# Optimization experiments

Measured on AMD Instinct MI355X. Metric: run time of the kernel, lower is better.

Reference implementation:

```python
import jax, jax.numpy as jnp
import numpy as np

EPS = 1e-08


def _center(K):
    # H K H with H = I - 11^T/n, expressed as O(n^2) double mean-subtraction
    rm = K.mean(axis=-1, keepdims=True)
    cm = K.mean(axis=-2, keepdims=True)
    tm = K.mean(axis=(-1, -2), keepdims=True)
    return K - rm - cm + tm


def setup_inputs() -> dict:
    key = jax.random.key(0)
    k1, k2 = jax.random.split(key)
    L, B, n, d = 5, 8, 1024, 64
    teacher = jax.random.normal(k1, (L, B, n, d), dtype=jnp.float32)
    student = jax.random.normal(k2, (L, B, n, d), dtype=jnp.float32)
    return {"teacher": teacher, "student": student}


def reference(teacher, student):
    # teacher, student: [L, B, n, d]  (internal=True, dim>=3 branch)
    cX = _center(jnp.einsum('lbnd,lbmd->lbnm', teacher, teacher))  # [L,B,n,n]
    cY = _center(jnp.einsum('lbnd,lbmd->lbnm', student, student))  # [L,B,n,n]
    hsic_xy = jnp.sum(cX * cY, axis=(-1, -2))  # [L,B]
    var_x = jnp.sqrt(jnp.sum(cX * cX, axis=(-1, -2)))  # [L,B]
    var_y = jnp.sqrt(jnp.sum(cY * cY, axis=(-1, -2)))  # [L,B]
    ratio = jnp.abs(hsic_xy / (var_x * var_y))  # [L,B]
    loss_per_layer = -jnp.log(ratio.mean(axis=-1) + EPS)  # [L]
    return loss_per_layer.mean()  # sum over layers / length
```

## Files before the change

### kernel.cpp

```cpp
#include <hip/hip_runtime.h>
#include <math.h>

#define LL 5
#define BB 8
#define NN 1024
#define DD 64
#define LB 40
#define SPLIT 16
#define KC (NN / SPLIT)
#define ZC (2 * DD)
#define NQ 3

#define GP_SHORTS (LB * SPLIT * NQ * 4096)
#define GP_FLOATS (GP_SHORTS / 2)
#define SP_OFF GP_FLOATS
#define ACC_OFF (GP_FLOATS + LB * SPLIT * ZC)

typedef short short8 __attribute__((ext_vector_type(8)));
typedef float floatx4 __attribute__((ext_vector_type(4)));

__device__ __forceinline__ unsigned short f2bf(float f) {
    union { float f; unsigned u; } v; v.f = f;
    const unsigned u = v.u;
    return (unsigned short)((u + 0x7FFFu + ((u >> 16) & 1u)) >> 16);
}
__device__ __forceinline__ float bf2f(unsigned short h) {
    union { unsigned u; float f; } v; v.u = ((unsigned)h) << 16; return v.f;
}
__device__ __forceinline__ float bflo(unsigned u) {
    union { unsigned u; float f; } v; v.u = u << 16; return v.f;
}
__device__ __forceinline__ float bfhi(unsigned u) {
    union { unsigned u; float f; } v; v.u = u & 0xFFFF0000u; return v.f;
}

__device__ __forceinline__ short8 read_frag(const short* Zt, int tbase, int lane, int k0) {
    const int c = tbase + (lane & 15);
    const int o = (k0 >> 3) + (lane >> 4);
    const int oct = (o ^ ((c + (c >> 4)) & 15)) & 7;
    return *(const short8*)(Zt + c * 64 + (oct << 3));
}

__global__ __launch_bounds__(256) void gram_kernel(const float* __restrict__ X,
                                                   const float* __restrict__ Y,
                                                   unsigned* __restrict__ Gp,
                                                   float* __restrict__ Sp) {
    __shared__ short Zt[ZC * KC];
    __shared__ float cscr[8][ZC];

    const int lb = blockIdx.y, nc = blockIdx.x, tid = threadIdx.x;
    const int r0 = nc * KC;
    const float4* X4 = (const float4*)(X + (size_t)lb * NN * DD);
    const float4* Y4 = (const float4*)(Y + (size_t)lb * NN * DD);

    const int col4 = tid & 31;
    const int rb = tid >> 5;
    float4 v[8];
#pragma unroll
    for (int m = 0; m < 8; ++m) {
        const int row = 8 * rb + m;
        v[m] = (col4 < 16) ? X4[(size_t)(r0 + row) * 16 + col4]
                           : Y4[(size_t)(r0 + row) * 16 + (col4 - 16)];
    }

#pragma unroll
    for (int e = 0; e < 4; ++e) {
        const int c = 4 * col4 + e;
        short8 w8;
        float cs = 0.f;
#pragma unroll
        for (int m = 0; m < 8; ++m) {
            const float fv = (e == 0) ? v[m].x : (e == 1) ? v[m].y : (e == 2) ? v[m].z : v[m].w;
            const unsigned short b = f2bf(fv);
            cs += bf2f(b);
            w8[m] = (short)b;
        }
        const int oct = (rb ^ ((c + (c >> 4)) & 15)) & 7;
        *(short8*)(Zt + c * 64 + (oct << 3)) = w8;
        cscr[rb][c] = cs;
    }
    __syncthreads();
    if (tid < ZC) {
        float s = 0.f;
#pragma unroll
        for (int g = 0; g < 8; ++g) s += cscr[g][tid];
        Sp[(lb * SPLIT + nc) * ZC + tid] = s;
    }

    const int lane = tid & 63, w = tid >> 6;
    const int jbeg = (w < 2) ? 0 : 4;

    floatx4 acc[2][8];
#pragma unroll
    for (int i = 0; i < 2; ++i)
#pragma unroll
        for (int j = 0; j < 8; ++j) acc[i][j] = (floatx4){0.f, 0.f, 0.f, 0.f};

#pragma unroll
    for (int k0 = 0; k0 < KC; k0 += 32) {
        short8 af[2], bfr[8];
#pragma unroll
        for (int i = 0; i < 2; ++i) af[i] = read_frag(Zt, (2 * w + i) * 16, lane, k0);
#pragma unroll
        for (int j = 0; j < 8; ++j)
            if (j >= jbeg) bfr[j] = read_frag(Zt, j * 16, lane, k0);
#pragma unroll
        for (int i = 0; i < 2; ++i)
#pragma unroll
            for (int j = 0; j < 8; ++j)
                if (j >= jbeg)
                    acc[i][j] = __builtin_amdgcn_mfma_f32_16x16x32_bf16(af[i], bfr[j], acc[i][j], 0, 0, 0);
    }

    unsigned* Gb = Gp + (size_t)(lb * SPLIT + nc) * (NQ * 2048);
    const int g = lane >> 4, cl = lane & 15;
#pragma unroll
    for (int i = 0; i < 2; ++i)
#pragma unroll
        for (int j = 0; j < 8; ++j) {
            if (j < jbeg) continue;
            const int slab = (w < 2) ? ((j < 4) ? 0 : 1) : 2;
            const int qrow0 = (w < 2 ? (2 * w + i) : (2 * (w - 2) + i)) * 16 + g * 4;
            const int qcol = (j & 3) * 16 + cl;
            const unsigned lo = (unsigned)f2bf(acc[i][j][0]) | ((unsigned)f2bf(acc[i][j][1]) << 16);
            const unsigned hi = (unsigned)f2bf(acc[i][j][2]) | ((unsigned)f2bf(acc[i][j][3]) << 16);
            Gb[slab * 2048 + (qrow0 >> 1) * 64 + qcol] = lo;
            Gb[slab * 2048 + ((qrow0 >> 1) + 1) * 64 + qcol] = hi;
        }
}

__global__ __launch_bounds__(256) void reduce_kernel(const unsigned* __restrict__ Gp,
                                                     const float* __restrict__ Sp,
                                                     float* __restrict__ Acc2) {
    const int b = blockIdx.x;
    const int lb = b / (NQ * 4);
    const int rem = b % (NQ * 4);
    const int q = rem >> 2, seg = rem & 3;
    const int tid = threadIdx.x;

    __shared__ float stot[ZC];
    __shared__ float red[4];

    if (tid < ZC) {
        float s = 0.f;
#pragma unroll
        for (int sp = 0; sp < SPLIT; ++sp) s += Sp[(lb * SPLIT + sp) * ZC + tid];
        stot[tid] = s;
    }
    __syncthreads();

    const int u0 = seg * 512 + tid * 2;
    const int rp = u0 >> 6;
    const int c0 = u0 & 63;

    float g00 = 0.f, g10 = 0.f, g01 = 0.f, g11 = 0.f;
#pragma unroll
    for (int sp = 0; sp < SPLIT; ++sp) {
        const uint2 p = *(const uint2*)&Gp[((size_t)(lb * SPLIT + sp) * NQ + q) * 2048 + u0];
        g00 += bflo(p.x); g10 += bfhi(p.x);
        g01 += bflo(p.y); g11 += bfhi(p.y);
    }
    const int rowbase = (q == 2) ? 64 : 0;
    const int colbase = (q == 0) ? 0 : 64;
    const float inv_n = 1.0f / (float)NN;
    const float sr0 = stot[rowbase + 2 * rp] * inv_n;
    const float sr1 = stot[rowbase + 2 * rp + 1] * inv_n;
    const float sc0 = stot[colbase + c0];
    const float sc1 = stot[colbase + c0 + 1];
    float sq = 0.f;
    { const float cv = g00 - sr0 * sc0; sq += cv * cv; }
    { const float cv = g10 - sr1 * sc0; sq += cv * cv; }
    { const float cv = g01 - sr0 * sc1; sq += cv * cv; }
    { const float cv = g11 - sr1 * sc1; sq += cv * cv; }

#pragma unroll
    for (int off = 32; off; off >>= 1) sq += __shfl_down(sq, off);
    const int wave = tid >> 6;
    if ((tid & 63) == 0) red[wave] = sq;
    __syncthreads();
    if (tid == 0)
        Acc2[lb * 12 + q * 4 + seg] = red[0] + red[1] + red[2] + red[3];
}

__global__ void final_kernel(const float* __restrict__ Acc2, float* __restrict__ out) {
    const int tid = threadIdx.x;
    float v = 0.0f;
    if (tid < LB) {
        float vxx = 0.f, hxy = 0.f, vyy = 0.f;
#pragma unroll
        for (int s = 0; s < 4; ++s) {
            vxx += Acc2[tid * 12 + s];
            hxy += Acc2[tid * 12 + 4 + s];
            vyy += Acc2[tid * 12 + 8 + s];
        }
        v = fabsf(hxy / (sqrtf(vxx) * sqrtf(vyy)));
    }
    v += __shfl_xor(v, 1);
    v += __shfl_xor(v, 2);
    v += __shfl_xor(v, 4);
    float loss = 0.0f;
#pragma unroll
    for (int l = 0; l < LL; ++l) {
        const float sl = __shfl(v, l * BB);
        loss += -logf(sl * (1.0f / (float)BB) + 1e-8f);
    }
    if (tid == 0) out[0] = loss * (1.0f / (float)LL);
}

extern "C" void kernel_launch(void* const* d_in, const int* in_sizes, int n_in,
                              void* d_out, int out_size, void* d_ws, size_t ws_size,
                              hipStream_t stream) {
    const float* teacher = (const float*)d_in[0];
    const float* student = (const float*)d_in[1];
    float* ws = (float*)d_ws;
    unsigned* Gp = (unsigned*)ws;
    float* Sp = ws + SP_OFF;
    float* Acc2 = ws + ACC_OFF;

    dim3 grid1(SPLIT, LB);
    gram_kernel<<<grid1, 256, 0, stream>>>(teacher, student, Gp, Sp);
    reduce_kernel<<<LB * NQ * 4, 256, 0, stream>>>(Gp, Sp, Acc2);
    final_kernel<<<1, 64, 0, stream>>>(Acc2, (float*)d_out);
}
```

Before: 78.99 us.

## Halve split count, store fp32 MFMA fragments, fold final kernel into reduce

```diff
diff --git a/kernel.cpp b/kernel.cpp
--- a/kernel.cpp
+++ b/kernel.cpp
@@ -6,15 +6,15 @@
 #define NN 1024
 #define DD 64
 #define LB 40
-#define SPLIT 16
-#define KC (NN / SPLIT)
-#define ZC (2 * DD)
-#define NQ 3
-
-#define GP_SHORTS (LB * SPLIT * NQ * 4096)
-#define GP_FLOATS (GP_SHORTS / 2)
-#define SP_OFF GP_FLOATS
-#define ACC_OFF (GP_FLOATS + LB * SPLIT * ZC)
+#define SPLIT 8
+#define KC 128
+#define ZC 128
+#define PF_PER 12288
+
+#define SP_OFF 0
+#define ACC_OFF (LB * SPLIT * ZC)
+#define CNT_OFF (ACC_OFF + LB * 3)
+#define P_OFF (ACC_OFF + 128)
 
 typedef short short8 __attribute__((ext_vector_type(8)));
 typedef float floatx4 __attribute__((ext_vector_type(4)));
@@ -27,31 +27,27 @@
 __device__ __forceinline__ float bf2f(unsigned short h) {
     union { unsigned u; float f; } v; v.u = ((unsigned)h) << 16; return v.f;
 }
-__device__ __forceinline__ float bflo(unsigned u) {
-    union { unsigned u; float f; } v; v.u = u << 16; return v.f;
-}
-__device__ __forceinline__ float bfhi(unsigned u) {
-    union { unsigned u; float f; } v; v.u = u & 0xFFFF0000u; return v.f;
-}
 
 __device__ __forceinline__ short8 read_frag(const short* Zt, int tbase, int lane, int k0) {
     const int c = tbase + (lane & 15);
     const int o = (k0 >> 3) + (lane >> 4);
-    const int oct = (o ^ ((c + (c >> 4)) & 15)) & 7;
-    return *(const short8*)(Zt + c * 64 + (oct << 3));
-}
-
-__global__ __launch_bounds__(256) void gram_kernel(const float* __restrict__ X,
+    const int oct = (o ^ ((c + (c >> 4)) & 15)) & 15;
+    return *(const short8*)(Zt + c * KC + (oct << 3));
+}
+
+__global__ __launch_bounds__(512) void gram_kernel(const float* __restrict__ X,
                                                    const float* __restrict__ Y,
-                                                   unsigned* __restrict__ Gp,
-                                                   float* __restrict__ Sp) {
+                                                   float* __restrict__ ws) {
     __shared__ short Zt[ZC * KC];
-    __shared__ float cscr[8][ZC];
-
-    const int lb = blockIdx.y, nc = blockIdx.x, tid = threadIdx.x;
-    const int r0 = nc * KC;
+    __shared__ float cscr[16][ZC];
+
+    const int lb = blockIdx.y, sp = blockIdx.x, tid = threadIdx.x;
+    const int r0 = sp * KC;
     const float4* X4 = (const float4*)(X + (size_t)lb * NN * DD);
     const float4* Y4 = (const float4*)(Y + (size_t)lb * NN * DD);
+
+    if (blockIdx.x == 0 && blockIdx.y == 0 && tid < 128)
+        ((unsigned*)(ws + ACC_OFF))[tid] = 0u;
 
     const int col4 = tid & 31;
     const int rb = tid >> 5;
@@ -75,136 +71,129 @@
             cs += bf2f(b);
             w8[m] = (short)b;
         }
-        const int oct = (rb ^ ((c + (c >> 4)) & 15)) & 7;
-        *(short8*)(Zt + c * 64 + (oct << 3)) = w8;
+        const int oct = (rb ^ ((c + (c >> 4)) & 15)) & 15;
+        *(short8*)(Zt + c * KC + (oct << 3)) = w8;
         cscr[rb][c] = cs;
     }
     __syncthreads();
     if (tid < ZC) {
         float s = 0.f;
 #pragma unroll
-        for (int g = 0; g < 8; ++g) s += cscr[g][tid];
-        Sp[(lb * SPLIT + nc) * ZC + tid] = s;
+        for (int g = 0; g < 16; ++g) s += cscr[g][tid];
+        ws[SP_OFF + (lb * SPLIT + sp) * ZC + tid] = s;
     }
 
     const int lane = tid & 63, w = tid >> 6;
-    const int jbeg = (w < 2) ? 0 : 4;
-
-    floatx4 acc[2][8];
-#pragma unroll
-    for (int i = 0; i < 2; ++i)
-#pragma unroll
-        for (int j = 0; j < 8; ++j) acc[i][j] = (floatx4){0.f, 0.f, 0.f, 0.f};
+    const int jbeg = (w < 4) ? 0 : 4;
+
+    floatx4 acc[8];
+#pragma unroll
+    for (int j = 0; j < 8; ++j) acc[j] = (floatx4){0.f, 0.f, 0.f, 0.f};
 
 #pragma unroll
     for (int k0 = 0; k0 < KC; k0 += 32) {
-        short8 af[2], bfr[8];
-#pragma unroll
-        for (int i = 0; i < 2; ++i) af[i] = read_frag(Zt, (2 * w + i) * 16, lane, k0);
+        const short8 af = read_frag(Zt, 16 * w, lane, k0);
+        short8 bfr[8];
 #pragma unroll
         for (int j = 0; j < 8; ++j)
-            if (j >= jbeg) bfr[j] = read_frag(Zt, j * 16, lane, k0);
-#pragma unroll
-        for (int i = 0; i < 2; ++i)
-#pragma unroll
-            for (int j = 0; j < 8; ++j)
-                if (j >= jbeg)
-                    acc[i][j] = __builtin_amdgcn_mfma_f32_16x16x32_bf16(af[i], bfr[j], acc[i][j], 0, 0, 0);
-    }
-
-    unsigned* Gb = Gp + (size_t)(lb * SPLIT + nc) * (NQ * 2048);
-    const int g = lane >> 4, cl = lane & 15;
-#pragma unroll
-    for (int i = 0; i < 2; ++i)
-#pragma unroll
-        for (int j = 0; j < 8; ++j) {
-            if (j < jbeg) continue;
-            const int slab = (w < 2) ? ((j < 4) ? 0 : 1) : 2;
-            const int qrow0 = (w < 2 ? (2 * w + i) : (2 * (w - 2) + i)) * 16 + g * 4;
-            const int qcol = (j & 3) * 16 + cl;
-            const unsigned lo = (unsigned)f2bf(acc[i][j][0]) | ((unsigned)f2bf(acc[i][j][1]) << 16);
-            const unsigned hi = (unsigned)f2bf(acc[i][j][2]) | ((unsigned)f2bf(acc[i][j][3]) << 16);
-            Gb[slab * 2048 + (qrow0 >> 1) * 64 + qcol] = lo;
-            Gb[slab * 2048 + ((qrow0 >> 1) + 1) * 64 + qcol] = hi;
-        }
-}
-
-__global__ __launch_bounds__(256) void reduce_kernel(const unsigned* __restrict__ Gp,
-                                                     const float* __restrict__ Sp,
-                                                     float* __restrict__ Acc2) {
+            if (j >= jbeg) bfr[j] = read_frag(Zt, 16 * j, lane, k0);
+#pragma unroll
+        for (int j = 0; j < 8; ++j)
+            if (j >= jbeg)
+                acc[j] = __builtin_amdgcn_mfma_f32_16x16x32_bf16(af, bfr[j], acc[j], 0, 0, 0);
+    }
+
+    float* Pb = ws + P_OFF + (size_t)(lb * SPLIT + sp) * PF_PER;
+#pragma unroll
+    for (int j = 0; j < 8; ++j) {
+        if (j < jbeg) continue;
+        const int q = (w < 4) ? ((j < 4) ? 0 : 1) : 2;
+        const int ti = (w < 4) ? w : (w - 4);
+        const int t = ti * 4 + (j & 3);
+        *(floatx4*)(Pb + ((q * 16 + t) * 64 + lane) * 4) = acc[j];
+    }
+}
+
+__global__ __launch_bounds__(256) void reduce_kernel(float* __restrict__ ws,
+                                                     float* __restrict__ out) {
     const int b = blockIdx.x;
-    const int lb = b / (NQ * 4);
-    const int rem = b % (NQ * 4);
+    const int lb = b / 12;
+    const int rem = b % 12;
     const int q = rem >> 2, seg = rem & 3;
     const int tid = threadIdx.x;
 
-    __shared__ float stot[ZC];
+    __shared__ float Sl[ZC];
     __shared__ float red[4];
+    __shared__ unsigned lastflag;
 
     if (tid < ZC) {
         float s = 0.f;
 #pragma unroll
-        for (int sp = 0; sp < SPLIT; ++sp) s += Sp[(lb * SPLIT + sp) * ZC + tid];
-        stot[tid] = s;
-    }
-    __syncthreads();
-
-    const int u0 = seg * 512 + tid * 2;
-    const int rp = u0 >> 6;
-    const int c0 = u0 & 63;
-
-    float g00 = 0.f, g10 = 0.f, g01 = 0.f, g11 = 0.f;
-#pragma unroll
-    for (int sp = 0; sp < SPLIT; ++sp) {
-        const uint2 p = *(const uint2*)&Gp[((size_t)(lb * SPLIT + sp) * NQ + q) * 2048 + u0];
-        g00 += bflo(p.x); g10 += bfhi(p.x);
-        g01 += bflo(p.y); g11 += bfhi(p.y);
-    }
+        for (int sp = 0; sp < SPLIT; ++sp)
+            s += ws[SP_OFF + (lb * SPLIT + sp) * ZC + tid];
+        Sl[tid] = s;
+    }
+    __syncthreads();
+
+    const int wv = tid >> 6, lane = tid & 63;
+    const int t = seg * 4 + wv;
+    const int ti = t >> 2, tj = t & 3;
+
+    const float* Pb = ws + P_OFF + (size_t)(lb * SPLIT) * PF_PER
+                    + ((q * 16 + t) * 64 + lane) * 4;
+    floatx4 sum = (floatx4){0.f, 0.f, 0.f, 0.f};
+#pragma unroll
+    for (int sp = 0; sp < SPLIT; ++sp)
+        sum += *(const floatx4*)(Pb + (size_t)sp * PF_PER);
+
     const int rowbase = (q == 2) ? 64 : 0;
     const int colbase = (q == 0) ? 0 : 64;
-    const float inv_n = 1.0f / (float)NN;
-    const float sr0 = stot[rowbase + 2 * rp] * inv_n;
-    const float sr1 = stot[rowbase + 2 * rp + 1] * inv_n;
-    const float sc0 = stot[colbase + c0];
-    const float sc1 = stot[colbase + c0 + 1];
+    const int R0 = rowbase + ti * 16 + (lane >> 4) * 4;
+    const int C = colbase + tj * 16 + (lane & 15);
+    const float sc = Sl[C] * (1.0f / (float)NN);
     float sq = 0.f;
-    { const float cv = g00 - sr0 * sc0; sq += cv * cv; }
-    { const float cv = g10 - sr1 * sc0; sq += cv * cv; }
-    { const float cv = g01 - sr0 * sc1; sq += cv * cv; }
-    { const float cv = g11 - sr1 * sc1; sq += cv * cv; }
+#pragma unroll
+    for (int r = 0; r < 4; ++r) {
+        const float cv = sum[r] - Sl[R0 + r] * sc;
+        sq += cv * cv;
+    }
 
 #pragma unroll
     for (int off = 32; off; off >>= 1) sq += __shfl_down(sq, off);
-    const int wave = tid >> 6;
-    if ((tid & 63) == 0) red[wave] = sq;
-    __syncthreads();
-    if (tid == 0)
-        Acc2[lb * 12 + q * 4 + seg] = red[0] + red[1] + red[2] + red[3];
-}
-
-__global__ void final_kernel(const float* __restrict__ Acc2, float* __restrict__ out) {
-    const int tid = threadIdx.x;
-    float v = 0.0f;
-    if (tid < LB) {
-        float vxx = 0.f, hxy = 0.f, vyy = 0.f;
-#pragma unroll
-        for (int s = 0; s < 4; ++s) {
-            vxx += Acc2[tid * 12 + s];
-            hxy += Acc2[tid * 12 + 4 + s];
-            vyy += Acc2[tid * 12 + 8 + s];
+    if (lane == 0) red[wv] = sq;
+    __syncthreads();
+
+    if (tid == 0) {
+        const float tot = red[0] + red[1] + red[2] + red[3];
+        atomicAdd(ws + ACC_OFF + lb * 3 + q, tot);
+        __threadfence();
+        unsigned* cnt = (unsigned*)(ws + CNT_OFF);
+        const unsigned old = atomicAdd(cnt, 1u);
+        lastflag = (old == (unsigned)(LB * 12 - 1)) ? 1u : 0u;
+    }
+    __syncthreads();
+
+    if (lastflag && tid < 64) {
+        __threadfence();
+        const float* Acc = ws + ACC_OFF;
+        float vr = 0.f;
+        if (tid < LB) {
+            const float vxx = __hip_atomic_load(Acc + tid * 3 + 0, __ATOMIC_RELAXED, __HIP_MEMORY_SCOPE_AGENT);
+            const float hxy = __hip_atomic_load(Acc + tid * 3 + 1, __ATOMIC_RELAXED, __HIP_MEMORY_SCOPE_AGENT);
+            const float vyy = __hip_atomic_load(Acc + tid * 3 + 2, __ATOMIC_RELAXED, __HIP_MEMORY_SCOPE_AGENT);
+            vr = fabsf(hxy / (sqrtf(vxx) * sqrtf(vyy)));
         }
-        v = fabsf(hxy / (sqrtf(vxx) * sqrtf(vyy)));
-    }
-    v += __shfl_xor(v, 1);
-    v += __shfl_xor(v, 2);
-    v += __shfl_xor(v, 4);
-    float loss = 0.0f;
-#pragma unroll
-    for (int l = 0; l < LL; ++l) {
-        const float sl = __shfl(v, l * BB);
-        loss += -logf(sl * (1.0f / (float)BB) + 1e-8f);
-    }
-    if (tid == 0) out[0] = loss * (1.0f / (float)LL);
+        vr += __shfl_xor(vr, 1);
+        vr += __shfl_xor(vr, 2);
+        vr += __shfl_xor(vr, 4);
+        float loss = 0.f;
+#pragma unroll
+        for (int l = 0; l < LL; ++l) {
+            const float sl = __shfl(vr, l * BB);
+            loss += -logf(sl * (1.0f / (float)BB) + 1e-8f);
+        }
+        if (tid == 0) out[0] = loss * (1.0f / (float)LL);
+    }
 }
 
 extern "C" void kernel_launch(void* const* d_in, const int* in_sizes, int n_in,
@@ -213,12 +202,8 @@
     const float* teacher = (const float*)d_in[0];
     const float* student = (const float*)d_in[1];
     float* ws = (float*)d_ws;
-    unsigned* Gp = (unsigned*)ws;
-    float* Sp = ws + SP_OFF;
-    float* Acc2 = ws + ACC_OFF;
 
     dim3 grid1(SPLIT, LB);
-    gram_kernel<<<grid1, 256, 0, stream>>>(teacher, student, Gp, Sp);
-    reduce_kernel<<<LB * NQ * 4, 256, 0, stream>>>(Gp, Sp, Acc2);
-    final_kernel<<<1, 64, 0, stream>>>(Acc2, (float*)d_out);
-}
+    gram_kernel<<<grid1, 512, 0, stream>>>(teacher, student, ws);
+    reduce_kernel<<<LB * 12, 256, 0, stream>>>(ws, (float*)d_out);
+}
```

Result: slower. 92.65 us (+17.3%).
